# Optimization experiments

Measured on AMD Instinct MI355X. Metric: run time of the kernel, lower is better.

Reference implementation:

```python
import jax, jax.numpy as jnp
import numpy as np

B = 64          # graphs per batch
NPG = 1024      # nodes per graph (equal-size graphs)
N = B * NPG
NF = 8          # node feature dim; voltage at index -3
MIN_DIST = 2.9
MAX_XY_EXP = 0.02
W_RECON, W_VOL, W_ELEC, W_COLL, W_FIELD = 1.0, 10.0, 50.0, 5.0, 2.0


def setup_inputs() -> dict:
    key = jax.random.key(0)
    k1, k2, k3, k4 = jax.random.split(key, 4)
    pred_coords = jax.random.normal(k1, (N, 3), dtype=jnp.float32) * 5.0
    true_coords = jax.random.normal(k2, (N, 3), dtype=jnp.float32) * 5.0
    original_coords = jax.random.normal(k3, (N, 3), dtype=jnp.float32) * 5.0
    node_features = jax.random.normal(k4, (N, NF), dtype=jnp.float32)
    batch_vector = jnp.repeat(jnp.arange(B, dtype=jnp.int64), NPG)
    return {"pred_coords": pred_coords, "true_coords": true_coords,
            "original_coords": original_coords, "node_features": node_features,
            "batch_vector": batch_vector}


def _relu(x):
    return jnp.maximum(x, 0.0)


def reference(pred_coords, true_coords, original_coords, node_features, batch_vector):
    # equal-size graphs -> to_dense_batch == reshape, mask all True
    p = pred_coords.reshape(B, NPG, 3)
    o = original_coords.reshape(B, NPG, 3)

    # --- reconstruction MSE ---
    recon = jnp.mean((pred_coords - true_coords) ** 2)

    # --- volume constraint: per-graph bbox expansion ratios ---
    pdims = p.max(axis=1) - p.min(axis=1)          # [B,3]
    odims = o.max(axis=1) - o.min(axis=1)          # [B,3]
    ratios = (pdims - odims) / (odims + 1e-8)
    xy_pen = _relu(ratios[:, :2] - MAX_XY_EXP).sum(axis=-1)
    z_pen = _relu(ratios[:, 2])
    volume = jnp.mean(xy_pen + 2.0 * z_pen)        # sum over graphs / B

    z = o[:, :, 2]                                  # [B,n]
    zmin = z.min(axis=1, keepdims=True)
    zmax = z.max(axis=1, keepdims=True)
    zr = zmax - zmin
    emask = (z <= zmin + 0.15 * zr) | (z >= zmax - 0.15 * zr)   # [B,n]
    cnt = emask.sum().astype(jnp.float32)
    diff2 = ((p - o) ** 2).sum(axis=-1)             # [B,n]
    electrode = (diff2 * emask).sum() / (cnt * 3.0)  # MSE over selected elements

    # --- anti-collapse: pairwise distances, off-diagonal relu(min_dist - d)^2 ---
    sq = (p * p).sum(axis=-1)                       # [B,n]
    d2 = sq[:, :, None] + sq[:, None, :] - 2.0 * jnp.einsum('bnd,bmd->bnm', p, p)
    d = jnp.sqrt(jnp.maximum(d2, 1e-12))            # [B,n,n]
    offdiag = 1.0 - jnp.eye(NPG, dtype=jnp.float32)
    viol2 = (_relu(MIN_DIST - d) ** 2) * offdiag
    collapse = jnp.mean(viol2.sum(axis=(1, 2)) / (NPG * (NPG - 1)))

    # --- field alignment: z center-of-mass vs voltage-dependent target ---
    v = node_features.reshape(B, NPG, NF)[:, 0, -3]  # first node's feature[-3]
    zp = p[:, :, 2]
    zcom = zp.mean(axis=1)
    zpmin = zp.min(axis=1)
    zpr = zp.max(axis=1) - zpmin
    znorm = (zcom - zpmin) / (zpr + 1e-8)
    target = jnp.where(v > 0, 0.6, 0.4)
    contrib = jnp.where(jnp.abs(v) >= 1e-6, (znorm - target) ** 2, 0.0)
    field = contrib.sum() / B

    total = (W_RECON * recon + W_VOL * volume + W_ELEC * electrode
             + W_COLL * collapse + W_FIELD * field)
    return (total, recon, volume, electrode, collapse, field)
```

## Files before the change

### kernel.cpp

```cpp
#include <hip/hip_runtime.h>
#include <math.h>

#define NB 64
#define NPG 1024
#define NFEAT 8
#define NTOT (NB * NPG)
#define TT 256

static constexpr float MIN_DIST = 2.9f;

#if __has_builtin(__builtin_amdgcn_sqrtf)
#define FAST_SQRT(x) __builtin_amdgcn_sqrtf(x)
#else
#define FAST_SQRT(x) sqrtf(x)
#endif

#define WS_STATS 0
#define WS_V     4096
#define WS_CNT   4160
#define WS_ELE   4224
#define WS_COLL  4288

__device__ __forceinline__ float waveSum(float v) {
#pragma unroll
  for (int o = 32; o > 0; o >>= 1) v += __shfl_down(v, o, 64);
  return v;
}
__device__ __forceinline__ float waveMin(float v) {
#pragma unroll
  for (int o = 32; o > 0; o >>= 1) v = fminf(v, __shfl_down(v, o, 64));
  return v;
}
__device__ __forceinline__ float waveMax(float v) {
#pragma unroll
  for (int o = 32; o > 0; o >>= 1) v = fmaxf(v, __shfl_down(v, o, 64));
  return v;
}

__global__ __launch_bounds__(256) void stats_partial(
    const float* __restrict__ pred, const float* __restrict__ tru,
    const float* __restrict__ orig, const float* __restrict__ feat,
    float* __restrict__ ws) {
  __shared__ float sh[14][4];
  const int blk = blockIdx.x;
  const int b = blk >> 2, q = blk & 3;
  const int tid = threadIdx.x;
  const int i = q * 256 + tid;
  const float* pb = pred + (size_t)b * NPG * 3;
  const float* tb = tru  + (size_t)b * NPG * 3;
  const float* ob = orig + (size_t)b * NPG * 3;

  float p0 = pb[i*3+0], p1 = pb[i*3+1], p2 = pb[i*3+2];
  float t0 = tb[i*3+0], t1 = tb[i*3+1], t2 = tb[i*3+2];
  float o0 = ob[i*3+0], o1 = ob[i*3+1], o2 = ob[i*3+2];
  float d0 = p0 - t0, d1 = p1 - t1, d2 = p2 - t2;
  float rec = d0*d0 + d1*d1 + d2*d2;

  float r[14];
  r[0]  = waveMin(p0); r[1]  = waveMin(p1); r[2]  = waveMin(p2);
  r[3]  = waveMax(p0); r[4]  = waveMax(p1); r[5]  = waveMax(p2);
  r[6]  = waveMin(o0); r[7]  = waveMin(o1); r[8]  = waveMin(o2);
  r[9]  = waveMax(o0); r[10] = waveMax(o1); r[11] = waveMax(o2);
  r[12] = waveSum(rec);
  r[13] = waveSum(p2);

  const int lane = tid & 63, wid = tid >> 6;
  if (lane == 0) {
#pragma unroll
    for (int k = 0; k < 14; k++) sh[k][wid] = r[k];
  }
  __syncthreads();
  if (tid == 0) {
    float* w = ws + WS_STATS + ((size_t)blk << 4);
#pragma unroll
    for (int k = 0; k < 3; k++) {
      w[k]     = fminf(fminf(sh[k][0],     sh[k][1]),     fminf(sh[k][2],     sh[k][3]));
      w[k + 3] = fmaxf(fmaxf(sh[k + 3][0], sh[k + 3][1]), fmaxf(sh[k + 3][2], sh[k + 3][3]));
      w[k + 6] = fminf(fminf(sh[k + 6][0], sh[k + 6][1]), fminf(sh[k + 6][2], sh[k + 6][3]));
      w[k + 9] = fmaxf(fmaxf(sh[k + 9][0], sh[k + 9][1]), fmaxf(sh[k + 9][2], sh[k + 9][3]));
    }
    w[12] = sh[12][0] + sh[12][1] + sh[12][2] + sh[12][3];
    w[13] = sh[13][0] + sh[13][1] + sh[13][2] + sh[13][3];
    if (q == 0) ws[WS_V + b] = feat[(size_t)b * NPG * NFEAT + (NFEAT - 3)];
  }
}

__global__ __launch_bounds__(256) void coll_elec(
    const float* __restrict__ pred, const float* __restrict__ orig,
    float* __restrict__ ws) {
  __shared__ float4 pts[TT];
  __shared__ float sred[4];
  __shared__ float se[2][4];
  const int x = blockIdx.x;
  const int b = x >> 4, s = x & 15;
  const int ic = s >> 2, jc = s & 3;
  const int tid = threadIdx.x;
  const float* pb = pred + (size_t)b * NPG * 3;

  const int j = jc * TT + tid;
  pts[tid] = make_float4(pb[j*3+0], pb[j*3+1], pb[j*3+2], 0.f);
  const int i = ic * TT + tid;
  const float px = pb[i*3+0], py = pb[i*3+1], pz = pb[i*3+2];
  __syncthreads();

  float acc = 0.f;
#pragma unroll 8
  for (int k = 0; k < TT; k++) {
    float4 pj = pts[k];
    float dx = px - pj.x, dy = py - pj.y, dz = pz - pj.z;
    float d2 = fmaf(dx, dx, fmaf(dy, dy, dz * dz));
    float d = FAST_SQRT(d2);
    float t = fmaxf(MIN_DIST - d, 0.f);
    acc = fmaf(t, t, acc);
  }
  if (ic == jc) acc -= MIN_DIST * MIN_DIST;
  acc = waveSum(acc);
  if ((tid & 63) == 0) sred[tid >> 6] = acc;

  float cnt = 0.f, el = 0.f;
  if (s == 0) {
    const float* ob = orig + (size_t)b * NPG * 3;
    float ozmin = INFINITY, ozmax = -INFINITY;
#pragma unroll
    for (int qq = 0; qq < 4; qq++) {
      const float* w = ws + WS_STATS + ((size_t)(b * 4 + qq) << 4);
      ozmin = fminf(ozmin, w[8]);
      ozmax = fmaxf(ozmax, w[11]);
    }
    const float zr = ozmax - ozmin;
    const float lo = ozmin + 0.15f * zr;
    const float hi = ozmax - 0.15f * zr;
#pragma unroll
    for (int kk = 0; kk < 4; kk++) {
      const int ii = kk * 256 + tid;
      float oz = ob[ii*3+2];
      if (oz <= lo || oz >= hi) {
        float e0 = pb[ii*3+0] - ob[ii*3+0];
        float e1 = pb[ii*3+1] - ob[ii*3+1];
        float e2 = pb[ii*3+2] - oz;
        cnt += 1.f;
        el += e0*e0 + e1*e1 + e2*e2;
      }
    }
    cnt = waveSum(cnt);
    el = waveSum(el);
    if ((tid & 63) == 0) { se[0][tid >> 6] = cnt; se[1][tid >> 6] = el; }
  }
  __syncthreads();
  if (tid == 0) {
    ws[WS_COLL + x] = sred[0] + sred[1] + sred[2] + sred[3];
    if (s == 0) {
      ws[WS_CNT + b] = se[0][0] + se[0][1] + se[0][2] + se[0][3];
      ws[WS_ELE + b] = se[1][0] + se[1][1] + se[1][2] + se[1][3];
    }
  }
}

__global__ __launch_bounds__(256) void final_kernel(
    const float* __restrict__ ws, float* __restrict__ out) {
  const int tid = threadIdx.x;
  __shared__ float shc[4];

  float c = 0.f;
  for (int k = tid; k < 1024; k += 256) c += ws[WS_COLL + k];
  c = waveSum(c);
  if ((tid & 63) == 0) shc[tid >> 6] = c;
  __syncthreads();

  if (tid < 64) {
    const int bb = tid;
    float pmn0 =  INFINITY, pmn1 =  INFINITY, pmn2 =  INFINITY;
    float pmx0 = -INFINITY, pmx1 = -INFINITY, pmx2 = -INFINITY;
    float omn0 =  INFINITY, omn1 =  INFINITY, omn2 =  INFINITY;
    float omx0 = -INFINITY, omx1 = -INFINITY, omx2 = -INFINITY;
    float rec = 0.f, zs = 0.f;
#pragma unroll
    for (int q = 0; q < 4; q++) {
      const float* w = ws + WS_STATS + ((size_t)(bb * 4 + q) << 4);
      pmn0 = fminf(pmn0, w[0]);  pmn1 = fminf(pmn1, w[1]);  pmn2 = fminf(pmn2, w[2]);
      pmx0 = fmaxf(pmx0, w[3]);  pmx1 = fmaxf(pmx1, w[4]);  pmx2 = fmaxf(pmx2, w[5]);
      omn0 = fminf(omn0, w[6]);  omn1 = fminf(omn1, w[7]);  omn2 = fminf(omn2, w[8]);
      omx0 = fmaxf(omx0, w[9]);  omx1 = fmaxf(omx1, w[10]); omx2 = fmaxf(omx2, w[11]);
      rec += w[12]; zs += w[13];
    }
    float pdx = pmx0 - pmn0, pdy = pmx1 - pmn1, pdz = pmx2 - pmn2;
    float odx = omx0 - omn0, ody = omx1 - omn1, odz = omx2 - omn2;
    float rx = (pdx - odx) / (odx + 1e-8f);
    float ry = (pdy - ody) / (ody + 1e-8f);
    float rz = (pdz - odz) / (odz + 1e-8f);
    float vol = fmaxf(rx - 0.02f, 0.f) + fmaxf(ry - 0.02f, 0.f) +
                2.f * fmaxf(rz, 0.f);

    float v = ws[WS_V + bb];
    float zcom = zs * (1.f / NPG);
    float znorm = (zcom - pmn2) / (pdz + 1e-8f);
    float target = (v > 0.f) ? 0.6f : 0.4f;
    float dd = znorm - target;
    float contrib = (fabsf(v) >= 1e-6f) ? dd * dd : 0.f;

    float cnt = ws[WS_CNT + bb];
    float el  = ws[WS_ELE + bb];

    vol = waveSum(vol);
    contrib = waveSum(contrib);
    rec = waveSum(rec);
    cnt = waveSum(cnt);
    el  = waveSum(el);

    if (tid == 0) {
      float ctot = shc[0] + shc[1] + shc[2] + shc[3];
      float o_recon  = rec / (float)(NTOT * 3);
      float o_volume = vol / (float)NB;
      float o_elec   = el / (cnt * 3.f);
      float o_coll   = ctot / ((float)NB * NPG * (NPG - 1));
      float o_field  = contrib / (float)NB;
      float total = 1.0f * o_recon + 10.0f * o_volume + 50.0f * o_elec +
                    5.0f * o_coll + 2.0f * o_field;
      out[0] = total;
      out[1] = o_recon;
      out[2] = o_volume;
      out[3] = o_elec;
      out[4] = o_coll;
      out[5] = o_field;
    }
  }
}

extern "C" void kernel_launch(void* const* d_in, const int* in_sizes, int n_in,
                              void* d_out, int out_size, void* d_ws, size_t ws_size,
                              hipStream_t stream) {
  const float* pred = (const float*)d_in[0];
  const float* tru  = (const float*)d_in[1];
  const float* orig = (const float*)d_in[2];
  const float* feat = (const float*)d_in[3];
  float* ws  = (float*)d_ws;
  float* out = (float*)d_out;

  stats_partial<<<256, 256, 0, stream>>>(pred, tru, orig, feat, ws);
  coll_elec<<<1024, 256, 0, stream>>>(pred, orig, ws);
  final_kernel<<<1, 256, 0, stream>>>(ws, out);
}
```

Baseline: 90.61 us.

## Exploit pairwise distance symmetry with upper-triangular tiles and fuse stats kernel

The collision term now uses only the upper-triangular 128x128 tile pairs (36 per graph), doubling off-diagonal tiles, which roughly halves the pairwise work. The separate stats kernel is folded into the first tile block of each graph, which computes bbox, recon and electrode sums serially over 1024 nodes. This removes one launch. The cost is that this one block per graph does extra serial work, and the smaller tiles reduce reuse.

```diff
diff --git a/kernel.cpp b/kernel.cpp
--- a/kernel.cpp
+++ b/kernel.cpp
@@ -5,7 +5,9 @@
 #define NPG 1024
 #define NFEAT 8
 #define NTOT (NB * NPG)
-#define TT 256
+#define TT 128
+#define NTILE 36
+#define NBLK (NB * NTILE)
 
 static constexpr float MIN_DIST = 2.9f;
 
@@ -16,10 +18,17 @@
 #endif
 
 #define WS_STATS 0
-#define WS_V     4096
-#define WS_CNT   4160
-#define WS_ELE   4224
-#define WS_COLL  4288
+#define WS_V     1024
+#define WS_CNT   1088
+#define WS_ELE   1152
+#define WS_COLL  1216
+
+__constant__ unsigned char ICT[NTILE] = {
+    0,0,0,0,0,0,0,0, 1,1,1,1,1,1,1, 2,2,2,2,2,2,
+    3,3,3,3,3, 4,4,4,4, 5,5,5, 6,6, 7};
+__constant__ unsigned char JCT[NTILE] = {
+    0,1,2,3,4,5,6,7, 1,2,3,4,5,6,7, 2,3,4,5,6,7,
+    3,4,5,6,7, 4,5,6,7, 5,6,7, 6,7, 7};
 
 __device__ __forceinline__ float waveSum(float v) {
 #pragma unroll
@@ -37,68 +46,25 @@
   return v;
 }
 
-__global__ __launch_bounds__(256) void stats_partial(
+__global__ __launch_bounds__(128) void main_kernel(
     const float* __restrict__ pred, const float* __restrict__ tru,
     const float* __restrict__ orig, const float* __restrict__ feat,
     float* __restrict__ ws) {
-  __shared__ float sh[14][4];
-  const int blk = blockIdx.x;
-  const int b = blk >> 2, q = blk & 3;
+  __shared__ float4 pts[TT];
+  __shared__ float scoll[2];
+  __shared__ float sst[16][2];
+  const int x = blockIdx.x;
+  const int b = x / NTILE;
+  const int s = x - b * NTILE;
+  const int ic = ICT[s], jc = JCT[s];
   const int tid = threadIdx.x;
-  const int i = q * 256 + tid;
+  const int wid = tid >> 6, lane = tid & 63;
   const float* pb = pred + (size_t)b * NPG * 3;
-  const float* tb = tru  + (size_t)b * NPG * 3;
-  const float* ob = orig + (size_t)b * NPG * 3;
-
-  float p0 = pb[i*3+0], p1 = pb[i*3+1], p2 = pb[i*3+2];
-  float t0 = tb[i*3+0], t1 = tb[i*3+1], t2 = tb[i*3+2];
-  float o0 = ob[i*3+0], o1 = ob[i*3+1], o2 = ob[i*3+2];
-  float d0 = p0 - t0, d1 = p1 - t1, d2 = p2 - t2;
-  float rec = d0*d0 + d1*d1 + d2*d2;
-
-  float r[14];
-  r[0]  = waveMin(p0); r[1]  = waveMin(p1); r[2]  = waveMin(p2);
-  r[3]  = waveMax(p0); r[4]  = waveMax(p1); r[5]  = waveMax(p2);
-  r[6]  = waveMin(o0); r[7]  = waveMin(o1); r[8]  = waveMin(o2);
-  r[9]  = waveMax(o0); r[10] = waveMax(o1); r[11] = waveMax(o2);
-  r[12] = waveSum(rec);
-  r[13] = waveSum(p2);
-
-  const int lane = tid & 63, wid = tid >> 6;
-  if (lane == 0) {
-#pragma unroll
-    for (int k = 0; k < 14; k++) sh[k][wid] = r[k];
-  }
-  __syncthreads();
-  if (tid == 0) {
-    float* w = ws + WS_STATS + ((size_t)blk << 4);
-#pragma unroll
-    for (int k = 0; k < 3; k++) {
-      w[k]     = fminf(fminf(sh[k][0],     sh[k][1]),     fminf(sh[k][2],     sh[k][3]));
-      w[k + 3] = fmaxf(fmaxf(sh[k + 3][0], sh[k + 3][1]), fmaxf(sh[k + 3][2], sh[k + 3][3]));
-      w[k + 6] = fminf(fminf(sh[k + 6][0], sh[k + 6][1]), fminf(sh[k + 6][2], sh[k + 6][3]));
-      w[k + 9] = fmaxf(fmaxf(sh[k + 9][0], sh[k + 9][1]), fmaxf(sh[k + 9][2], sh[k + 9][3]));
-    }
-    w[12] = sh[12][0] + sh[12][1] + sh[12][2] + sh[12][3];
-    w[13] = sh[13][0] + sh[13][1] + sh[13][2] + sh[13][3];
-    if (q == 0) ws[WS_V + b] = feat[(size_t)b * NPG * NFEAT + (NFEAT - 3)];
-  }
-}
-
-__global__ __launch_bounds__(256) void coll_elec(
-    const float* __restrict__ pred, const float* __restrict__ orig,
-    float* __restrict__ ws) {
-  __shared__ float4 pts[TT];
-  __shared__ float sred[4];
-  __shared__ float se[2][4];
-  const int x = blockIdx.x;
-  const int b = x >> 4, s = x & 15;
-  const int ic = s >> 2, jc = s & 3;
-  const int tid = threadIdx.x;
-  const float* pb = pred + (size_t)b * NPG * 3;
-
-  const int j = jc * TT + tid;
-  pts[tid] = make_float4(pb[j*3+0], pb[j*3+1], pb[j*3+2], 0.f);
+
+  {
+    const int j = jc * TT + tid;
+    pts[tid] = make_float4(pb[j*3+0], pb[j*3+1], pb[j*3+2], 0.f);
+  }
   const int i = ic * TT + tid;
   const float px = pb[i*3+0], py = pb[i*3+1], pz = pb[i*3+2];
   __syncthreads();
@@ -114,25 +80,71 @@
     acc = fmaf(t, t, acc);
   }
   if (ic == jc) acc -= MIN_DIST * MIN_DIST;
+  else          acc += acc;
   acc = waveSum(acc);
-  if ((tid & 63) == 0) sred[tid >> 6] = acc;
-
-  float cnt = 0.f, el = 0.f;
+  if (lane == 0) scoll[wid] = acc;
+  __syncthreads();
+  if (tid == 0) ws[WS_COLL + x] = scoll[0] + scoll[1];
+
   if (s == 0) {
+    const float* tb = tru  + (size_t)b * NPG * 3;
     const float* ob = orig + (size_t)b * NPG * 3;
-    float ozmin = INFINITY, ozmax = -INFINITY;
-#pragma unroll
-    for (int qq = 0; qq < 4; qq++) {
-      const float* w = ws + WS_STATS + ((size_t)(b * 4 + qq) << 4);
-      ozmin = fminf(ozmin, w[8]);
-      ozmax = fmaxf(ozmax, w[11]);
-    }
-    const float zr = ozmax - ozmin;
-    const float lo = ozmin + 0.15f * zr;
-    const float hi = ozmax - 0.15f * zr;
-#pragma unroll
-    for (int kk = 0; kk < 4; kk++) {
-      const int ii = kk * 256 + tid;
+    float pmn0 =  INFINITY, pmn1 =  INFINITY, pmn2 =  INFINITY;
+    float pmx0 = -INFINITY, pmx1 = -INFINITY, pmx2 = -INFINITY;
+    float omn0 =  INFINITY, omn1 =  INFINITY, omn2 =  INFINITY;
+    float omx0 = -INFINITY, omx1 = -INFINITY, omx2 = -INFINITY;
+    float rec = 0.f, zps = 0.f;
+    for (int k = 0; k < 8; k++) {
+      const int ii = k * TT + tid;
+      float p0 = pb[ii*3+0], p1 = pb[ii*3+1], p2 = pb[ii*3+2];
+      float t0 = tb[ii*3+0], t1 = tb[ii*3+1], t2 = tb[ii*3+2];
+      float o0 = ob[ii*3+0], o1 = ob[ii*3+1], o2 = ob[ii*3+2];
+      pmn0 = fminf(pmn0, p0); pmx0 = fmaxf(pmx0, p0);
+      pmn1 = fminf(pmn1, p1); pmx1 = fmaxf(pmx1, p1);
+      pmn2 = fminf(pmn2, p2); pmx2 = fmaxf(pmx2, p2);
+      omn0 = fminf(omn0, o0); omx0 = fmaxf(omx0, o0);
+      omn1 = fminf(omn1, o1); omx1 = fmaxf(omx1, o1);
+      omn2 = fminf(omn2, o2); omx2 = fmaxf(omx2, o2);
+      float d0 = p0 - t0, d1 = p1 - t1, d2 = p2 - t2;
+      rec += d0*d0 + d1*d1 + d2*d2;
+      zps += p2;
+    }
+    float r[14];
+    r[0]  = waveMin(pmn0); r[1]  = waveMin(pmn1); r[2]  = waveMin(pmn2);
+    r[3]  = waveMax(pmx0); r[4]  = waveMax(pmx1); r[5]  = waveMax(pmx2);
+    r[6]  = waveMin(omn0); r[7]  = waveMin(omn1); r[8]  = waveMin(omn2);
+    r[9]  = waveMax(omx0); r[10] = waveMax(omx1); r[11] = waveMax(omx2);
+    r[12] = waveSum(rec);
+    r[13] = waveSum(zps);
+    if (lane == 0) {
+#pragma unroll
+      for (int q = 0; q < 14; q++) sst[q][wid] = r[q];
+    }
+    __syncthreads();
+    if (tid == 0) {
+      float* w = ws + WS_STATS + ((size_t)b << 4);
+      float c[14];
+#pragma unroll
+      for (int q = 0; q < 3; q++) {
+        c[q]     = fminf(sst[q][0],     sst[q][1]);
+        c[q + 3] = fmaxf(sst[q + 3][0], sst[q + 3][1]);
+        c[q + 6] = fminf(sst[q + 6][0], sst[q + 6][1]);
+        c[q + 9] = fmaxf(sst[q + 9][0], sst[q + 9][1]);
+      }
+      c[12] = sst[12][0] + sst[12][1];
+      c[13] = sst[13][0] + sst[13][1];
+#pragma unroll
+      for (int q = 0; q < 14; q++) w[q] = c[q];
+      float zr = c[11] - c[8];
+      sst[14][0] = c[8]  + 0.15f * zr;
+      sst[15][0] = c[11] - 0.15f * zr;
+      ws[WS_V + b] = feat[(size_t)b * NPG * NFEAT + (NFEAT - 3)];
+    }
+    __syncthreads();
+    const float lo = sst[14][0], hi = sst[15][0];
+    float cnt = 0.f, el = 0.f;
+    for (int k = 0; k < 8; k++) {
+      const int ii = k * TT + tid;
       float oz = ob[ii*3+2];
       if (oz <= lo || oz >= hi) {
         float e0 = pb[ii*3+0] - ob[ii*3+0];
@@ -143,15 +155,12 @@
       }
     }
     cnt = waveSum(cnt);
-    el = waveSum(el);
-    if ((tid & 63) == 0) { se[0][tid >> 6] = cnt; se[1][tid >> 6] = el; }
-  }
-  __syncthreads();
-  if (tid == 0) {
-    ws[WS_COLL + x] = sred[0] + sred[1] + sred[2] + sred[3];
-    if (s == 0) {
-      ws[WS_CNT + b] = se[0][0] + se[0][1] + se[0][2] + se[0][3];
-      ws[WS_ELE + b] = se[1][0] + se[1][1] + se[1][2] + se[1][3];
+    el  = waveSum(el);
+    if (lane == 0) { sst[0][wid] = cnt; sst[1][wid] = el; }
+    __syncthreads();
+    if (tid == 0) {
+      ws[WS_CNT + b] = sst[0][0] + sst[0][1];
+      ws[WS_ELE + b] = sst[1][0] + sst[1][1];
     }
   }
 }
@@ -162,44 +171,33 @@
   __shared__ float shc[4];
 
   float c = 0.f;
-  for (int k = tid; k < 1024; k += 256) c += ws[WS_COLL + k];
+  for (int k = tid; k < NBLK; k += 256) c += ws[WS_COLL + k];
   c = waveSum(c);
   if ((tid & 63) == 0) shc[tid >> 6] = c;
   __syncthreads();
 
   if (tid < 64) {
-    const int bb = tid;
-    float pmn0 =  INFINITY, pmn1 =  INFINITY, pmn2 =  INFINITY;
-    float pmx0 = -INFINITY, pmx1 = -INFINITY, pmx2 = -INFINITY;
-    float omn0 =  INFINITY, omn1 =  INFINITY, omn2 =  INFINITY;
-    float omx0 = -INFINITY, omx1 = -INFINITY, omx2 = -INFINITY;
-    float rec = 0.f, zs = 0.f;
-#pragma unroll
-    for (int q = 0; q < 4; q++) {
-      const float* w = ws + WS_STATS + ((size_t)(bb * 4 + q) << 4);
-      pmn0 = fminf(pmn0, w[0]);  pmn1 = fminf(pmn1, w[1]);  pmn2 = fminf(pmn2, w[2]);
-      pmx0 = fmaxf(pmx0, w[3]);  pmx1 = fmaxf(pmx1, w[4]);  pmx2 = fmaxf(pmx2, w[5]);
-      omn0 = fminf(omn0, w[6]);  omn1 = fminf(omn1, w[7]);  omn2 = fminf(omn2, w[8]);
-      omx0 = fmaxf(omx0, w[9]);  omx1 = fmaxf(omx1, w[10]); omx2 = fmaxf(omx2, w[11]);
-      rec += w[12]; zs += w[13];
-    }
-    float pdx = pmx0 - pmn0, pdy = pmx1 - pmn1, pdz = pmx2 - pmn2;
-    float odx = omx0 - omn0, ody = omx1 - omn1, odz = omx2 - omn2;
+    const float* w = ws + WS_STATS + ((size_t)tid << 4);
+    float pmn2 = w[2];
+    float pdx = w[3] - w[0], pdy = w[4] - w[1], pdz = w[5] - w[2];
+    float odx = w[9] - w[6], ody = w[10] - w[7], odz = w[11] - w[8];
+    float rec = w[12], zs = w[13];
+
     float rx = (pdx - odx) / (odx + 1e-8f);
     float ry = (pdy - ody) / (ody + 1e-8f);
     float rz = (pdz - odz) / (odz + 1e-8f);
     float vol = fmaxf(rx - 0.02f, 0.f) + fmaxf(ry - 0.02f, 0.f) +
                 2.f * fmaxf(rz, 0.f);
 
-    float v = ws[WS_V + bb];
+    float v = ws[WS_V + tid];
     float zcom = zs * (1.f / NPG);
     float znorm = (zcom - pmn2) / (pdz + 1e-8f);
     float target = (v > 0.f) ? 0.6f : 0.4f;
     float dd = znorm - target;
     float contrib = (fabsf(v) >= 1e-6f) ? dd * dd : 0.f;
 
-    float cnt = ws[WS_CNT + bb];
-    float el  = ws[WS_ELE + bb];
+    float cnt = ws[WS_CNT + tid];
+    float el  = ws[WS_ELE + tid];
 
     vol = waveSum(vol);
     contrib = waveSum(contrib);
@@ -236,7 +234,6 @@
   float* ws  = (float*)d_ws;
   float* out = (float*)d_out;
 
-  stats_partial<<<256, 256, 0, stream>>>(pred, tru, orig, feat, ws);
-  coll_elec<<<1024, 256, 0, stream>>>(pred, orig, ws);
+  main_kernel<<<NBLK, 128, 0, stream>>>(pred, tru, orig, feat, ws);
   final_kernel<<<1, 256, 0, stream>>>(ws, out);
 }
```

Measured after the change: 83.43 us. 7.9% less time.
